# Kernel optimization log

Hardware: AMD Instinct MI355X
Metric: run time of the kernel (lower is better)

## Reference

```python
import jax, jax.numpy as jnp
import numpy as np

HEADS = 16
DIM_HEAD = 64
QUERY_DIM = 1024
INNER_DIM = HEADS * DIM_HEAD  # 1024
SCALE = DIM_HEAD ** -0.5


def setup_inputs() -> dict:
    key = jax.random.key(0)
    ks = jax.random.split(key, 6)
    B, S = 2, 2048
    hidden_states = jax.random.normal(ks[0], (B, S, QUERY_DIM), dtype=jnp.float32)
    # torch Linear weights are [out, in]; store transposed [in, out] for x @ W
    w_q = jax.random.normal(ks[1], (QUERY_DIM, INNER_DIM), dtype=jnp.float32) * (QUERY_DIM ** -0.5)
    w_k = jax.random.normal(ks[2], (QUERY_DIM, INNER_DIM), dtype=jnp.float32) * (QUERY_DIM ** -0.5)
    w_v = jax.random.normal(ks[3], (QUERY_DIM, INNER_DIM), dtype=jnp.float32) * (QUERY_DIM ** -0.5)
    w_o = jax.random.normal(ks[4], (INNER_DIM, QUERY_DIM), dtype=jnp.float32) * (INNER_DIM ** -0.5)
    b_o = jax.random.normal(ks[5], (QUERY_DIM,), dtype=jnp.float32) * 0.01
    return {"hidden_states": hidden_states, "w_q": w_q, "w_k": w_k, "w_v": w_v, "w_o": w_o, "b_o": b_o}


def reference(hidden_states, w_q, w_k, w_v, w_o, b_o):
    B, S, _ = hidden_states.shape
    # QKV projections (context = hidden_states, i.e. self-attention)
    q = (hidden_states @ w_q).reshape(B, S, HEADS, DIM_HEAD)
    k = (hidden_states @ w_k).reshape(B, S, HEADS, DIM_HEAD)
    v = (hidden_states @ w_v).reshape(B, S, HEADS, DIM_HEAD)
    # scaled dot-product attention; scores materialized as [B, H, S, S]
    scores = jnp.einsum("bqhd,bkhd->bhqk", q, k) * SCALE
    probs = jax.nn.softmax(scores, axis=-1)
    out = jnp.einsum("bhqk,bkhd->bqhd", probs, v).reshape(B, S, INNER_DIM)
    return out @ w_o + b_o
```

## Files before the change

### kernel.cpp

```cpp
#include <hip/hip_runtime.h>
#include <cstdint>
#include <cstddef>

typedef unsigned short u16;
typedef unsigned int u32;
typedef __bf16 bf16x8 __attribute__((ext_vector_type(8)));
typedef float f32x4 __attribute__((ext_vector_type(4)));
typedef float f32x16 __attribute__((ext_vector_type(16)));
typedef u32 u32x2 __attribute__((ext_vector_type(2)));
typedef u32 u32x4 __attribute__((ext_vector_type(4)));

#define AS1 __attribute__((address_space(1)))
#define AS3 __attribute__((address_space(3)))

__device__ __forceinline__ void gld16(const u16* g, u16* l) {
  __builtin_amdgcn_global_load_lds((const AS1 void*)(const void*)g,
                                   (AS3 void*)(void*)l, 16, 0, 0);
}

__device__ __forceinline__ u16 f2bf(float f) {
  union { float f; unsigned u; } x; x.f = f;
  return (u16)((x.u + 0x7fffu + ((x.u >> 16) & 1u)) >> 16);
}

__device__ __forceinline__ f32x16 zf16() {
  f32x16 v;
#pragma unroll
  for (int i = 0; i < 16; ++i) v[i] = 0.f;
  return v;
}

__device__ __forceinline__ bf16x8 mk8(u32x2 a, u32x2 b) {
  union { u32x4 u; bf16x8 v; } x;
  x.u[0] = a[0]; x.u[1] = a[1]; x.u[2] = b[0]; x.u[3] = b[1];
  return x.v;
}

__global__ void k_prep(const float* __restrict__ X,
                       const float* __restrict__ wq, const float* __restrict__ wk,
                       const float* __restrict__ wv, const float* __restrict__ wo,
                       u16* __restrict__ Xb, u16* __restrict__ Wqkv, u16* __restrict__ Wot) {
  const int z = blockIdx.z;
  if (z == 4) {
    int bid = blockIdx.y * 32 + blockIdx.x;
    int tid = threadIdx.y * 32 + threadIdx.x;
#pragma unroll
    for (int k = 0; k < 4; ++k) {
      int i = bid * 1024 + k * 256 + tid;
      float4 v = reinterpret_cast<const float4*>(X)[i];
      ushort4 o;
      o.x = f2bf(v.x); o.y = f2bf(v.y); o.z = f2bf(v.z); o.w = f2bf(v.w);
      reinterpret_cast<ushort4*>(Xb)[i] = o;
    }
    return;
  }
  __shared__ float t[32][33];
  const float* in = (z == 0) ? wq : (z == 1) ? wk : (z == 2) ? wv : wo;
  u16* out = (z < 3) ? (Wqkv + (size_t)z * 1048576) : Wot;
  int bx = blockIdx.x * 32, by = blockIdx.y * 32;
  int tx = threadIdx.x, ty = threadIdx.y;
#pragma unroll
  for (int j = 0; j < 32; j += 8)
    t[ty + j][tx] = in[(size_t)(by + ty + j) * 1024 + bx + tx];
  __syncthreads();
#pragma unroll
  for (int j = 0; j < 32; j += 8)
    out[(size_t)(bx + ty + j) * 1024 + by + tx] = f2bf(t[tx][ty + j]);
}

__global__ __launch_bounds__(256) void k_gemm_qkv(
    const u16* __restrict__ Xb,
    const u16* __restrict__ Wt,
    u16* __restrict__ Qb,
    u16* __restrict__ Kb,
    u16* __restrict__ Vt) {
  __shared__ __align__(16) u16 As[128][32];
  __shared__ __align__(16) u16 Bs[128][32];
  const int tid = threadIdx.x;
  const int w = tid >> 6, l = tid & 63;
  const int bm = blockIdx.x * 128;
  const int bn = blockIdx.y * 128;
  const int wm = (w >> 1) * 64, wn = (w & 1) * 64;
  const int lm = l & 15, lg = l >> 4;

  f32x4 acc[4][4];
#pragma unroll
  for (int i = 0; i < 4; ++i)
#pragma unroll
    for (int j = 0; j < 4; ++j) acc[i][j] = f32x4{0.f, 0.f, 0.f, 0.f};

  const int srow = w * 16 + (l >> 2);
  const int scol = (l & 3) * 8;
  for (int k0 = 0; k0 < 1024; k0 += 32) {
#pragma unroll
    for (int j = 0; j < 2; ++j) {
      gld16(Xb + (size_t)(bm + j * 64 + srow) * 1024 + k0 + scol, &As[j * 64 + w * 16][0]);
      gld16(Wt + (size_t)(bn + j * 64 + srow) * 1024 + k0 + scol, &Bs[j * 64 + w * 16][0]);
    }
    __syncthreads();
    bf16x8 af[4], bfr[4];
#pragma unroll
    for (int mt = 0; mt < 4; ++mt)
      af[mt] = *reinterpret_cast<const bf16x8*>(&As[wm + mt * 16 + lm][lg * 8]);
#pragma unroll
    for (int nt = 0; nt < 4; ++nt)
      bfr[nt] = *reinterpret_cast<const bf16x8*>(&Bs[wn + nt * 16 + lm][lg * 8]);
#pragma unroll
    for (int mt = 0; mt < 4; ++mt)
#pragma unroll
      for (int nt = 0; nt < 4; ++nt)
        acc[mt][nt] = __builtin_amdgcn_mfma_f32_16x16x32_bf16(af[mt], bfr[nt], acc[mt][nt], 0, 0, 0);
    __syncthreads();
  }
#pragma unroll
  for (int nt = 0; nt < 4; ++nt) {
    int gc = bn + wn + nt * 16 + lm;
    int which = gc >> 10, jc = gc & 1023, h = jc >> 6, d = jc & 63;
#pragma unroll
    for (int mt = 0; mt < 4; ++mt) {
#pragma unroll
      for (int r = 0; r < 4; ++r) {
        int gr = bm + wm + mt * 16 + lg * 4 + r;
        int b = gr >> 11, s = gr & 2047;
        float v = acc[mt][nt][r];
        size_t bh = (size_t)(b * 16 + h);
        if (which == 0)      Qb[(bh * 2048 + s) * 64 + d] = f2bf(v * 0.18033688f);
        else if (which == 1) Kb[(bh * 2048 + s) * 64 + d] = f2bf(v);
        else                 Vt[(bh * 64 + d) * 2048 + s] = f2bf(v);
      }
    }
  }
}

__global__ __launch_bounds__(256) void k_attn(
    const u16* __restrict__ Qb, const u16* __restrict__ Kb,
    const u16* __restrict__ Vt, u16* __restrict__ Ab) {
  __shared__ __align__(16) u16 Ks[2][64][64];
  __shared__ __align__(16) u16 Vs[2][64][64];
  const int tid = threadIdx.x, w = tid >> 6, l = tid & 63;
  const int lm = l & 31, hi = l >> 5;
  const int kx = lm & 7;
  const int bh = blockIdx.x;
  const int q0 = blockIdx.y * 128 + w * 32;
  const u16* Qh = Qb + (size_t)bh * 2048 * 64;
  const u16* Kh = Kb + (size_t)bh * 2048 * 64;
  const u16* Vh = Vt + (size_t)bh * 64 * 2048;

  bf16x8 qf[4];
#pragma unroll
  for (int c = 0; c < 4; ++c)
    qf[c] = *reinterpret_cast<const bf16x8*>(&Qh[(size_t)(q0 + lm) * 64 + 16 * c + 8 * hi]);

  bf16x8 onesf;
#pragma unroll
  for (int i = 0; i < 8; ++i) onesf[i] = (lm == 0) ? (__bf16)1.0f : (__bf16)0.0f;

  f32x16 o0a = zf16(), o0b = zf16(), o1a = zf16(), o1b = zf16(), o2 = zf16();

  const int sr8 = l >> 3;
  const int sg = l & 7;

#pragma unroll
  for (int j = 0; j < 2; ++j) {
    int row = w * 16 + j * 8 + sr8;
    int g = sg ^ (row & 7);
    gld16(Kh + (size_t)row * 64 + 8 * g, &Ks[0][w * 16 + j * 8][0]);
    gld16(Vh + (size_t)row * 2048 + 8 * g, &Vs[0][w * 16 + j * 8][0]);
  }
  __syncthreads();

  for (int t = 0; t < 32; ++t) {
    const int cur = t & 1, nxt = cur ^ 1;

    if (t < 31) {
      const int kvn = (t + 1) * 64;
#pragma unroll
      for (int j = 0; j < 2; ++j) {
        int row = w * 16 + j * 8 + sr8;
        int g = sg ^ (row & 7);
        gld16(Kh + (size_t)(kvn + row) * 64 + 8 * g, &Ks[nxt][w * 16 + j * 8][0]);
        gld16(Vh + (size_t)row * 2048 + kvn + 8 * g, &Vs[nxt][w * 16 + j * 8][0]);
      }
    }

    const u16* Kc = &Ks[cur][0][0];
    f32x16 st0 = zf16(), st1 = zf16();
    __builtin_amdgcn_s_setprio(1);
#pragma unroll
    for (int c = 0; c < 4; ++c) {
      bf16x8 kf0 = *reinterpret_cast<const bf16x8*>(Kc + (size_t)lm * 64 + 8 * ((2 * c + hi) ^ kx));
      st0 = __builtin_amdgcn_mfma_f32_32x32x16_bf16(kf0, qf[c], st0, 0, 0, 0);
    }
#pragma unroll
    for (int c = 0; c < 4; ++c) {
      bf16x8 kf1 = *reinterpret_cast<const bf16x8*>(Kc + (size_t)(32 + lm) * 64 + 8 * ((2 * c + hi) ^ kx));
      st1 = __builtin_amdgcn_mfma_f32_32x32x16_bf16(kf1, qf[c], st1, 0, 0, 0);
    }
    __builtin_amdgcn_s_setprio(0);

    bf16x8 pf[2][2];
#pragma unroll
    for (int j = 0; j < 2; ++j)
#pragma unroll
      for (int ii = 0; ii < 8; ++ii) {
        pf[0][j][ii] = (__bf16)exp2f(st0[8 * j + ii]);
        pf[1][j][ii] = (__bf16)exp2f(st1[8 * j + ii]);
      }

    const u16* Vc = &Vs[cur][0][0];
    __builtin_amdgcn_s_setprio(1);
#pragma unroll
    for (int j = 0; j < 2; ++j) {
      int Ga = 2 * j;
      u32x2 a0 = *reinterpret_cast<const u32x2*>(Vc + (size_t)lm * 64 + 8 * (Ga ^ kx) + 4 * hi);
      u32x2 a1 = *reinterpret_cast<const u32x2*>(Vc + (size_t)lm * 64 + 8 * ((Ga + 1) ^ kx) + 4 * hi);
      u32x2 b0 = *reinterpret_cast<const u32x2*>(Vc + (size_t)(32 + lm) * 64 + 8 * (Ga ^ kx) + 4 * hi);
      u32x2 b1 = *reinterpret_cast<const u32x2*>(Vc + (size_t)(32 + lm) * 64 + 8 * ((Ga + 1) ^ kx) + 4 * hi);
      o0a = __builtin_amdgcn_mfma_f32_32x32x16_bf16(pf[0][j], mk8(a0, a1), o0a, 0, 0, 0);
      o1a = __builtin_amdgcn_mfma_f32_32x32x16_bf16(pf[0][j], mk8(b0, b1), o1a, 0, 0, 0);
      o2  = __builtin_amdgcn_mfma_f32_32x32x16_bf16(pf[0][j], onesf, o2, 0, 0, 0);
    }
#pragma unroll
    for (int j = 0; j < 2; ++j) {
      int Ga = 4 + 2 * j;
      u32x2 a0 = *reinterpret_cast<const u32x2*>(Vc + (size_t)lm * 64 + 8 * (Ga ^ kx) + 4 * hi);
      u32x2 a1 = *reinterpret_cast<const u32x2*>(Vc + (size_t)lm * 64 + 8 * ((Ga + 1) ^ kx) + 4 * hi);
      u32x2 b0 = *reinterpret_cast<const u32x2*>(Vc + (size_t)(32 + lm) * 64 + 8 * (Ga ^ kx) + 4 * hi);
      u32x2 b1 = *reinterpret_cast<const u32x2*>(Vc + (size_t)(32 + lm) * 64 + 8 * ((Ga + 1) ^ kx) + 4 * hi);
      o0b = __builtin_amdgcn_mfma_f32_32x32x16_bf16(pf[1][j], mk8(a0, a1), o0b, 0, 0, 0);
      o1b = __builtin_amdgcn_mfma_f32_32x32x16_bf16(pf[1][j], mk8(b0, b1), o1b, 0, 0, 0);
      o2  = __builtin_amdgcn_mfma_f32_32x32x16_bf16(pf[1][j], onesf, o2, 0, 0, 0);
    }
    __builtin_amdgcn_s_setprio(0);

    __syncthreads();
  }

  f32x16 o0 = o0a + o0b;
  f32x16 o1 = o1a + o1b;
  const int b = bh >> 4, h = bh & 15;
  const int src = hi << 5;
#pragma unroll
  for (int r = 0; r < 16; ++r) {
    int cr = (r & 3) + 8 * (r >> 2) + 4 * hi;
    float s = __shfl(o2[r], src);
    float inv = 1.0f / s;
    size_t ro = ((size_t)(b * 2048 + q0 + cr)) * 1024 + h * 64;
    Ab[ro + lm]      = f2bf(o0[r] * inv);
    Ab[ro + 32 + lm] = f2bf(o1[r] * inv);
  }
}

__global__ __launch_bounds__(256) void k_gemm_out(
    const u16* __restrict__ Ab,
    const u16* __restrict__ Wot,
    const float* __restrict__ bias, float* __restrict__ out) {
  __shared__ __align__(16) u16 As[128][32];
  __shared__ __align__(16) u16 Bs[128][32];
  const int tid = threadIdx.x;
  const int w = tid >> 6, l = tid & 63;
  const int bm = blockIdx.x * 128;
  const int bn = blockIdx.y * 128;
  const int wm = (w >> 1) * 64, wn = (w & 1) * 64;
  const int lm = l & 15, lg = l >> 4;

  f32x4 acc[4][4];
#pragma unroll
  for (int i = 0; i < 4; ++i)
#pragma unroll
    for (int j = 0; j < 4; ++j) acc[i][j] = f32x4{0.f, 0.f, 0.f, 0.f};

  const int srow = w * 16 + (l >> 2);
  const int scol = (l & 3) * 8;
  for (int k0 = 0; k0 < 1024; k0 += 32) {
#pragma unroll
    for (int j = 0; j < 2; ++j) {
      gld16(Ab  + (size_t)(bm + j * 64 + srow) * 1024 + k0 + scol, &As[j * 64 + w * 16][0]);
      gld16(Wot + (size_t)(bn + j * 64 + srow) * 1024 + k0 + scol, &Bs[j * 64 + w * 16][0]);
    }
    __syncthreads();
    bf16x8 af[4], bfr[4];
#pragma unroll
    for (int mt = 0; mt < 4; ++mt)
      af[mt] = *reinterpret_cast<const bf16x8*>(&As[wm + mt * 16 + lm][lg * 8]);
#pragma unroll
    for (int nt = 0; nt < 4; ++nt)
      bfr[nt] = *reinterpret_cast<const bf16x8*>(&Bs[wn + nt * 16 + lm][lg * 8]);
#pragma unroll
    for (int mt = 0; mt < 4; ++mt)
#pragma unroll
      for (int nt = 0; nt < 4; ++nt)
        acc[mt][nt] = __builtin_amdgcn_mfma_f32_16x16x32_bf16(af[mt], bfr[nt], acc[mt][nt], 0, 0, 0);
    __syncthreads();
  }
#pragma unroll
  for (int nt = 0; nt < 4; ++nt) {
    int gc = bn + wn + nt * 16 + lm;
    float bv = bias[gc];
#pragma unroll
    for (int mt = 0; mt < 4; ++mt) {
#pragma unroll
      for (int r = 0; r < 4; ++r) {
        int gr = bm + wm + mt * 16 + lg * 4 + r;
        out[(size_t)gr * 1024 + gc] = acc[mt][nt][r] + bv;
      }
    }
  }
}

extern "C" void kernel_launch(void* const* d_in, const int* in_sizes, int n_in,
                              void* d_out, int out_size, void* d_ws, size_t ws_size,
                              hipStream_t stream) {
  const float* X  = (const float*)d_in[0];
  const float* wq = (const float*)d_in[1];
  const float* wk = (const float*)d_in[2];
  const float* wv = (const float*)d_in[3];
  const float* wo = (const float*)d_in[4];
  const float* bo = (const float*)d_in[5];
  float* out = (float*)d_out;

  char* ws = (char*)d_ws;
  u16* Xb   = (u16*)(ws);
  u16* Wqkv = (u16*)(ws + (size_t)(8u  << 20));
  u16* Wot  = (u16*)(ws + (size_t)(14u << 20));
  u16* Qb   = (u16*)(ws + (size_t)(16u << 20));
  u16* Kb   = (u16*)(ws + (size_t)(24u << 20));
  u16* Vt   = (u16*)(ws + (size_t)(32u << 20));
  u16* Ab   = (u16*)(ws + (size_t)(40u << 20));

  k_prep<<<dim3(32, 32, 5), dim3(32, 8), 0, stream>>>(X, wq, wk, wv, wo, Xb, Wqkv, Wot);
  k_gemm_qkv<<<dim3(32, 24), 256, 0, stream>>>(Xb, Wqkv, Qb, Kb, Vt);
  k_attn<<<dim3(32, 16), 256, 0, stream>>>(Qb, Kb, Vt, Ab);
  k_gemm_out<<<dim3(32, 8), 256, 0, stream>>>(Ab, Wot, bo, out);
}
```

Before: 132.3 us.

## Split attention over two KV halves and merge partial outputs in a new kernel

The attention kernel now splits the 2048-key sequence into two halves along a new grid z dimension. Each block writes unnormalized bf16 partial outputs and per-row softmax denominators. A new merge kernel adds the two partials, divides by the combined denominator and writes the head-interleaved activation that the output GEMM consumes. This doubles the number of attention blocks to improve CU occupancy and latency hiding, at the cost of an extra launch, extra global traffic and bf16 rounding of the unnormalized partials; dead workspace regions are reused for the new buffers.

Result: slower. 140.2 us (+6.0%).

```diff
diff --git a/kernel.cpp b/kernel.cpp
--- a/kernel.cpp
+++ b/kernel.cpp
@@ -21,6 +21,10 @@
 __device__ __forceinline__ u16 f2bf(float f) {
   union { float f; unsigned u; } x; x.f = f;
   return (u16)((x.u + 0x7fffu + ((x.u >> 16) & 1u)) >> 16);
+}
+
+__device__ __forceinline__ float bf2f(u16 u) {
+  union { u32 i; float f; } x; x.i = ((u32)u) << 16; return x.f;
 }
 
 __device__ __forceinline__ f32x16 zf16() {
@@ -134,7 +138,9 @@
 
 __global__ __launch_bounds__(256) void k_attn(
     const u16* __restrict__ Qb, const u16* __restrict__ Kb,
-    const u16* __restrict__ Vt, u16* __restrict__ Ab) {
+    const u16* __restrict__ Vt,
+    u16* __restrict__ Opb,
+    float* __restrict__ lsums) {
   __shared__ __align__(16) u16 Ks[2][64][64];
   __shared__ __align__(16) u16 Vs[2][64][64];
   const int tid = threadIdx.x, w = tid >> 6, l = tid & 63;
@@ -142,9 +148,10 @@
   const int kx = lm & 7;
   const int bh = blockIdx.x;
   const int q0 = blockIdx.y * 128 + w * 32;
+  const int z = blockIdx.z;
   const u16* Qh = Qb + (size_t)bh * 2048 * 64;
-  const u16* Kh = Kb + (size_t)bh * 2048 * 64;
-  const u16* Vh = Vt + (size_t)bh * 64 * 2048;
+  const u16* Kh = Kb + ((size_t)bh * 2048 + z * 1024) * 64;
+  const u16* Vh = Vt + (size_t)bh * 64 * 2048 + z * 1024;
 
   bf16x8 qf[4];
 #pragma unroll
@@ -169,10 +176,10 @@
   }
   __syncthreads();
 
-  for (int t = 0; t < 32; ++t) {
+  for (int t = 0; t < 16; ++t) {
     const int cur = t & 1, nxt = cur ^ 1;
 
-    if (t < 31) {
+    if (t < 15) {
       const int kvn = (t + 1) * 64;
 #pragma unroll
       for (int j = 0; j < 2; ++j) {
@@ -238,17 +245,42 @@
 
   f32x16 o0 = o0a + o0b;
   f32x16 o1 = o1a + o1b;
-  const int b = bh >> 4, h = bh & 15;
-  const int src = hi << 5;
+  const size_t robase = ((size_t)z * 32 + bh) * 2048 + q0;
+  if (lm == 0) {
+#pragma unroll
+    for (int r = 0; r < 16; ++r) {
+      int cr = (r & 3) + 8 * (r >> 2) + 4 * hi;
+      lsums[robase + cr] = o2[r];
+    }
+  }
 #pragma unroll
   for (int r = 0; r < 16; ++r) {
     int cr = (r & 3) + 8 * (r >> 2) + 4 * hi;
-    float s = __shfl(o2[r], src);
-    float inv = 1.0f / s;
-    size_t ro = ((size_t)(b * 2048 + q0 + cr)) * 1024 + h * 64;
-    Ab[ro + lm]      = f2bf(o0[r] * inv);
-    Ab[ro + 32 + lm] = f2bf(o1[r] * inv);
-  }
+    size_t ro = (robase + cr) * 64;
+    Opb[ro + lm]      = f2bf(o0[r]);
+    Opb[ro + 32 + lm] = f2bf(o1[r]);
+  }
+}
+
+__global__ __launch_bounds__(256) void k_merge(
+    const u16* __restrict__ Opb, const float* __restrict__ lsums,
+    u16* __restrict__ Ab) {
+  int idx = blockIdx.x * 256 + threadIdx.x;
+  int d8 = idx & 7, q = (idx >> 3) & 2047, bh = idx >> 14;
+  size_t r0 = (size_t)bh * 2048 + q;
+  size_t r1 = (size_t)(32 + bh) * 2048 + q;
+  float inv = 1.0f / (lsums[r0] + lsums[r1]);
+  u32x4 a0 = *reinterpret_cast<const u32x4*>(&Opb[r0 * 64 + d8 * 8]);
+  u32x4 a1 = *reinterpret_cast<const u32x4*>(&Opb[r1 * 64 + d8 * 8]);
+  u32x4 o;
+#pragma unroll
+  for (int j = 0; j < 4; ++j) {
+    float lo = (bf2f((u16)(a0[j] & 0xffff)) + bf2f((u16)(a1[j] & 0xffff))) * inv;
+    float hb = (bf2f((u16)(a0[j] >> 16))    + bf2f((u16)(a1[j] >> 16)))    * inv;
+    o[j] = (u32)f2bf(lo) | ((u32)f2bf(hb) << 16);
+  }
+  int b = bh >> 4, h = bh & 15;
+  *reinterpret_cast<u32x4*>(&Ab[((size_t)b * 2048 + q) * 1024 + h * 64 + d8 * 8]) = o;
 }
 
 __global__ __launch_bounds__(256) void k_gemm_out(
@@ -320,16 +352,19 @@
   float* out = (float*)d_out;
 
   char* ws = (char*)d_ws;
-  u16* Xb   = (u16*)(ws);
-  u16* Wqkv = (u16*)(ws + (size_t)(8u  << 20));
-  u16* Wot  = (u16*)(ws + (size_t)(14u << 20));
-  u16* Qb   = (u16*)(ws + (size_t)(16u << 20));
-  u16* Kb   = (u16*)(ws + (size_t)(24u << 20));
-  u16* Vt   = (u16*)(ws + (size_t)(32u << 20));
-  u16* Ab   = (u16*)(ws + (size_t)(40u << 20));
+  u16*   Xb    = (u16*)(ws);
+  u16*   Wqkv  = (u16*)(ws + (size_t)(8u  << 20));
+  u16*   Wot   = (u16*)(ws + (size_t)(14u << 20));
+  u16*   Qb    = (u16*)(ws + (size_t)(16u << 20));
+  u16*   Kb    = (u16*)(ws + (size_t)(24u << 20));
+  u16*   Vt    = (u16*)(ws + (size_t)(32u << 20));
+  u16*   Opb   = (u16*)(ws + (size_t)(40u << 20));
+  float* lsums = (float*)(ws + (size_t)(8u << 20));
+  u16*   Ab    = (u16*)(ws);
 
   k_prep<<<dim3(32, 32, 5), dim3(32, 8), 0, stream>>>(X, wq, wk, wv, wo, Xb, Wqkv, Wot);
   k_gemm_qkv<<<dim3(32, 24), 256, 0, stream>>>(Xb, Wqkv, Qb, Kb, Vt);
-  k_attn<<<dim3(32, 16), 256, 0, stream>>>(Qb, Kb, Vt, Ab);
+  k_attn<<<dim3(32, 16, 2), 256, 0, stream>>>(Qb, Kb, Vt, Opb, lsums);
+  k_merge<<<2048, 256, 0, stream>>>(Opb, lsums, Ab);
   k_gemm_out<<<dim3(32, 8), 256, 0, stream>>>(Ab, Wot, bo, out);
 }
```

## Triple-buffer K/V tiles in attention with partial vmcnt waits

Applied to the files above, without the earlier changes.

The attention kernel moves from double to triple buffering of the K and V shared-memory tiles. It now prefetches two tiles ahead and uses explicit s_waitcnt vmcnt(4) plus raw s_barrier in place of __syncthreads, so loads for tile t+2 stay in flight while tile t+1 becomes ready. The goal is to hide global-to-LDS latency better and drop the full memory drain at each iteration barrier. Shared memory rises from 32KB to 48KB per block, which may reduce occupancy.

Result: no change. 134.3 us (+1.5%).

```diff
diff --git a/kernel.cpp b/kernel.cpp
--- a/kernel.cpp
+++ b/kernel.cpp
@@ -135,8 +135,8 @@
 __global__ __launch_bounds__(256) void k_attn(
     const u16* __restrict__ Qb, const u16* __restrict__ Kb,
     const u16* __restrict__ Vt, u16* __restrict__ Ab) {
-  __shared__ __align__(16) u16 Ks[2][64][64];
-  __shared__ __align__(16) u16 Vs[2][64][64];
+  __shared__ __align__(16) u16 Ks[3][64][64];
+  __shared__ __align__(16) u16 Vs[3][64][64];
   const int tid = threadIdx.x, w = tid >> 6, l = tid & 63;
   const int lm = l & 31, hi = l >> 5;
   const int kx = lm & 7;
@@ -160,29 +160,27 @@
   const int sr8 = l >> 3;
   const int sg = l & 7;
 
-#pragma unroll
-  for (int j = 0; j < 2; ++j) {
-    int row = w * 16 + j * 8 + sr8;
-    int g = sg ^ (row & 7);
-    gld16(Kh + (size_t)row * 64 + 8 * g, &Ks[0][w * 16 + j * 8][0]);
-    gld16(Vh + (size_t)row * 2048 + 8 * g, &Vs[0][w * 16 + j * 8][0]);
-  }
-  __syncthreads();
-
+#define STAGE(tile, buf)                                                        \
+  {                                                                             \
+    const int kvn_ = (tile) * 64;                                               \
+    _Pragma("unroll")                                                           \
+    for (int j = 0; j < 2; ++j) {                                               \
+      int row_ = w * 16 + j * 8 + sr8;                                          \
+      int g_ = sg ^ (row_ & 7);                                                 \
+      gld16(Kh + (size_t)(kvn_ + row_) * 64 + 8 * g_, &Ks[buf][w * 16 + j * 8][0]); \
+      gld16(Vh + (size_t)row_ * 2048 + kvn_ + 8 * g_, &Vs[buf][w * 16 + j * 8][0]); \
+    }                                                                           \
+  }
+
+  STAGE(0, 0);
+  STAGE(1, 1);
+  asm volatile("s_waitcnt vmcnt(4)" ::: "memory");
+  __builtin_amdgcn_sched_barrier(0);
+  __builtin_amdgcn_s_barrier();
+  __builtin_amdgcn_sched_barrier(0);
+
+  int cur = 0;
   for (int t = 0; t < 32; ++t) {
-    const int cur = t & 1, nxt = cur ^ 1;
-
-    if (t < 31) {
-      const int kvn = (t + 1) * 64;
-#pragma unroll
-      for (int j = 0; j < 2; ++j) {
-        int row = w * 16 + j * 8 + sr8;
-        int g = sg ^ (row & 7);
-        gld16(Kh + (size_t)(kvn + row) * 64 + 8 * g, &Ks[nxt][w * 16 + j * 8][0]);
-        gld16(Vh + (size_t)row * 2048 + kvn + 8 * g, &Vs[nxt][w * 16 + j * 8][0]);
-      }
-    }
-
     const u16* Kc = &Ks[cur][0][0];
     f32x16 st0 = zf16(), st1 = zf16();
     __builtin_amdgcn_s_setprio(1);
@@ -232,9 +230,22 @@
       o2  = __builtin_amdgcn_mfma_f32_32x32x16_bf16(pf[1][j], onesf, o2, 0, 0, 0);
     }
     __builtin_amdgcn_s_setprio(0);
-
-    __syncthreads();
-  }
+    __builtin_amdgcn_sched_barrier(0);
+
+    if (t < 30) {
+      int nb = cur + 2; if (nb >= 3) nb -= 3;
+      STAGE(t + 2, nb);
+      asm volatile("s_waitcnt vmcnt(4)" ::: "memory");
+    } else {
+      asm volatile("s_waitcnt vmcnt(0)" ::: "memory");
+    }
+    __builtin_amdgcn_sched_barrier(0);
+    __builtin_amdgcn_s_barrier();
+    __builtin_amdgcn_sched_barrier(0);
+
+    cur = (cur == 2) ? 0 : cur + 1;
+  }
+#undef STAGE
 
   f32x16 o0 = o0a + o0b;
   f32x16 o1 = o1a + o1b;
```
